# Kernel tuning notes

Measured on AMD Instinct MI355X. Metric: run time of the kernel, lower is better.

Reference implementation:

```python
import jax, jax.numpy as jnp
import numpy as np

K_NEIGS = 3
M_PROB = 1.0
EPS = 1e-12


def _gen_G_single(ft):
    """Build normalized hypergraph Laplacian G [N,N] from node coords ft [N,3].

    Mirrors construct_H_with_KNN (is_probH=True, m_prob=1) + generate_G_from_H
    from the HGNN reference code: per-center KNN hyperedges with probabilistic
    incidence exp(-d^2/(m_prob*avg_d)^2), then G = Dv^-1/2 H De^-1 H^T Dv^-1/2.
    """
    N = ft.shape[0]
    # squared pairwise Euclidean distances [N,N]
    sq_norm = jnp.sum(ft * ft, axis=1)
    sq = jnp.maximum(sq_norm[:, None] + sq_norm[None, :] - 2.0 * ft @ ft.T, 0.0)
    dist = jnp.sqrt(sq + EPS)
    avg_dis = jnp.mean(dist, axis=1)  # per-center mean distance [N]
    # K nearest neighbors per center (self is always included: sq[c,c]=0)
    neg_sq, idx = jax.lax.top_k(-sq, K_NEIGS)  # [N,K]
    # prob incidence: exp(-d^2 / (m_prob*avg)^2); neg_sq = -d^2
    vals = jnp.exp(neg_sq / (M_PROB * avg_dis[:, None]) ** 2)  # [N,K]
    # H[node, edge]: column c holds the K neighbors of center c
    H = jnp.zeros((N, N), ft.dtype).at[idx, jnp.arange(N)[:, None]].set(vals)
    de = jnp.sum(H, axis=0)              # edge degrees [N]
    dv = jnp.sum(H, axis=1)              # vertex degrees [N]
    inv_de = 1.0 / de
    dv2 = dv ** -0.5
    HW = H * inv_de[None, :]
    G = (dv2[:, None] * (HW @ H.T)) * dv2[None, :]
    return G


def reference(x, W1, b1, Wc, bc):
    # gen_G: per-batch hypergraph G [B,N,N]
    G = jax.vmap(_gen_G_single)(x)
    # HGNN_conv with both args = G: out = G @ (G @ W1 + b1)  -> [B,N,H1]
    f = jnp.matmul(G, jnp.matmul(G, W1) + b1)
    # max-pool over nodes, then classifier
    f = jnp.max(f, axis=1)               # [B,H1]
    return f @ Wc + bc                   # [B,class_num]


def setup_inputs() -> dict:
    key = jax.random.key(0)
    k1, k2, k3, k4, k5 = jax.random.split(key, 5)
    B, N, H1, C = 4, 2048, 128, 8
    x = jax.random.normal(k1, (B, N, 3), dtype=jnp.float32)
    W1 = jax.random.normal(k2, (N, H1), dtype=jnp.float32) / np.sqrt(N)
    b1 = jax.random.normal(k3, (H1,), dtype=jnp.float32) * 0.01
    Wc = jax.random.normal(k4, (H1, C), dtype=jnp.float32) / np.sqrt(H1)
    bc = jax.random.normal(k5, (C,), dtype=jnp.float32) * 0.01
    return {"x": x, "W1": W1, "b1": b1, "Wc": Wc, "bc": bc}
```

## Files before the change

kernel.cpp:

```cpp
#include <hip/hip_runtime.h>
#include <math.h>

#define NN 2048
#define BB 4
#define HD 128
#define CNUM 8
#define WPB 4
#define CAP 64
#define CAPG 128
#define NPB 4

typedef unsigned long long u64;

__device__ __forceinline__ u64 pack_key(float sq, int j) {
    return ((u64)__float_as_uint(sq) << 32) | (unsigned)j;
}
__device__ __forceinline__ void ins3(u64 k, u64& k0, u64& k1, u64& k2) {
    u64 a = k  < k2 ? k  : k2;
    u64 b = k0 > a  ? k0 : a;
    k0    = k0 < a  ? k0 : a;
    k2    = k1 > b  ? k1 : b;
    k1    = k1 < b  ? k1 : b;
}

__global__ void k_prep(const float* __restrict__ x, float4* __restrict__ pts) {
    const int t = blockIdx.x * 256 + threadIdx.x;
    const float a = x[3 * t], c = x[3 * t + 1], d = x[3 * t + 2];
    pts[t] = make_float4(a, c, d, a * a + c * c + d * d);
}

__global__ __launch_bounds__(256) void k_dist(
        const float4* __restrict__ pts,
        int* __restrict__ idx, float* __restrict__ vals,
        float* __restrict__ de, float* __restrict__ dv,
        int* __restrict__ cnt, int2* __restrict__ rev) {
    const int b = blockIdx.y;
    const float4* pb = pts + b * NN;
    const int wave = threadIdx.x >> 6;
    const int lane = threadIdx.x & 63;
    const int i = blockIdx.x * WPB + wave;
    const float4 ci = pb[i];
    u64 k0 = ~0ull, k1 = ~0ull, k2 = ~0ull;
    float dsA = 0.f, dsB = 0.f;
    for (int t = lane; t < NN; t += 256) {
        const float4 pa = pb[t];
        const float4 pv = pb[t + 64];
        const float4 pc = pb[t + 128];
        const float4 pd = pb[t + 192];
        const float qa = fmaxf(ci.w + pa.w - 2.0f * (ci.x * pa.x + ci.y * pa.y + ci.z * pa.z), 0.0f);
        const float qb = fmaxf(ci.w + pv.w - 2.0f * (ci.x * pv.x + ci.y * pv.y + ci.z * pv.z), 0.0f);
        const float qc = fmaxf(ci.w + pc.w - 2.0f * (ci.x * pc.x + ci.y * pc.y + ci.z * pc.z), 0.0f);
        const float qd = fmaxf(ci.w + pd.w - 2.0f * (ci.x * pd.x + ci.y * pd.y + ci.z * pd.z), 0.0f);
        dsA += __builtin_amdgcn_sqrtf(qa + 1e-12f) + __builtin_amdgcn_sqrtf(qc + 1e-12f);
        dsB += __builtin_amdgcn_sqrtf(qb + 1e-12f) + __builtin_amdgcn_sqrtf(qd + 1e-12f);
        ins3(pack_key(qa, t),       k0, k1, k2);
        ins3(pack_key(qb, t + 64),  k0, k1, k2);
        ins3(pack_key(qc, t + 128), k0, k1, k2);
        ins3(pack_key(qd, t + 192), k0, k1, k2);
    }
    float dsum = dsA + dsB;
    for (int off = 32; off > 0; off >>= 1) {
        const u64 o0 = __shfl_xor(k0, off);
        const u64 o1 = __shfl_xor(k1, off);
        const u64 o2 = __shfl_xor(k2, off);
        dsum += __shfl_xor(dsum, off);
        ins3(o0, k0, k1, k2);
        ins3(o1, k0, k1, k2);
        ins3(o2, k0, k1, k2);
    }
    if (lane == 0) {
        const float s0 = __uint_as_float((unsigned)(k0 >> 32));
        const float s1 = __uint_as_float((unsigned)(k1 >> 32));
        const float s2 = __uint_as_float((unsigned)(k2 >> 32));
        const int   i0 = (int)(k0 & 0xffffffffu);
        const int   i1 = (int)(k1 & 0xffffffffu);
        const int   i2 = (int)(k2 & 0xffffffffu);
        const float avg = dsum * (1.0f / NN);
        const float inva2 = 1.0f / (avg * avg);
        const float v0 = expf(-s0 * inva2);
        const float v1 = expf(-s1 * inva2);
        const float v2 = expf(-s2 * inva2);
        const int base = (b * NN + i) * 3;
        idx[base] = i0; idx[base + 1] = i1; idx[base + 2] = i2;
        vals[base] = v0; vals[base + 1] = v1; vals[base + 2] = v2;
        de[b * NN + i] = v0 + v1 + v2;
        atomicAdd(&dv[b * NN + i0], v0);
        atomicAdd(&dv[b * NN + i1], v1);
        atomicAdd(&dv[b * NN + i2], v2);
        const int p0 = atomicAdd(&cnt[b * NN + i0], 1);
        if (p0 < CAP) rev[((size_t)(b * NN + i0)) * CAP + p0] = make_int2(i, __float_as_int(v0));
        const int p1 = atomicAdd(&cnt[b * NN + i1], 1);
        if (p1 < CAP) rev[((size_t)(b * NN + i1)) * CAP + p1] = make_int2(i, __float_as_int(v1));
        const int p2 = atomicAdd(&cnt[b * NN + i2], 1);
        if (p2 < CAP) rev[((size_t)(b * NN + i2)) * CAP + p2] = make_int2(i, __float_as_int(v2));
    }
}

__global__ void k_gbuild(const int* __restrict__ idx, const float* __restrict__ vals,
                         const float* __restrict__ de, const float* __restrict__ dv,
                         const int* __restrict__ cnt, const int2* __restrict__ rev,
                         int2* __restrict__ glist, int* __restrict__ gn) {
    const int b = blockIdx.y;
    const int i = blockIdx.x * 256 + threadIdx.x;
    const int ni = b * NN + i;
    const int cn = min(cnt[ni], CAP);
    const float wi = rsqrtf(dv[ni]);
    int m = 0;
    for (int s = 0; s < cn; ++s) {
        const int2 r = rev[(size_t)ni * CAP + s];
        const int e = r.x;
        const float coef = wi * __int_as_float(r.y) / de[b * NN + e];
        const int eb = (b * NN + e) * 3;
        #pragma unroll
        for (int t = 0; t < 3; ++t) {
            const int j = idx[eb + t];
            const float gv = coef * vals[eb + t] * rsqrtf(dv[b * NN + j]);
            if (m < CAPG) glist[(size_t)ni * CAPG + m] = make_int2(j, __float_as_int(gv));
            ++m;
        }
    }
    gn[ni] = min(m, CAPG);
}

__global__ __launch_bounds__(256) void k_conv1(
        const float* __restrict__ W1, const float* __restrict__ b1,
        const int2* __restrict__ glist, const int* __restrict__ gn,
        float* __restrict__ f1) {
    const int b = blockIdx.y;
    const int i = blockIdx.x * 2 + (threadIdx.x >> 7);
    const int h = threadIdx.x & (HD - 1);
    const int ni = b * NN + i;
    const int n = gn[ni];
    const int2* gl = glist + (size_t)ni * CAPG;
    float acc = b1[h];
    int2 cur = gl[0];
    for (int s = 0; s < n; ++s) {
        const int2 nxt = gl[min(s + 1, n - 1)];
        acc += __int_as_float(cur.y) * W1[cur.x * HD + h];
        cur = nxt;
    }
    f1[(size_t)ni * HD + h] = acc;
}

__global__ __launch_bounds__(256) void k_conv2(
        const int2* __restrict__ glist, const int* __restrict__ gn,
        const float* __restrict__ f1, unsigned* __restrict__ pmaxK) {
    __shared__ float smx[2][HD];
    const int b = blockIdx.y;
    const int sub = threadIdx.x >> 7;
    const int h = threadIdx.x & (HD - 1);
    float mx = -INFINITY;
    for (int t = 0; t < NPB / 2; ++t) {
        const int i = blockIdx.x * NPB + t * 2 + sub;
        const int ni = b * NN + i;
        const int n = gn[ni];
        const int2* gl = glist + (size_t)ni * CAPG;
        float acc = 0.f;
        int2 cur = gl[0];
        for (int s = 0; s < n; ++s) {
            const int2 nxt = gl[min(s + 1, n - 1)];
            acc += __int_as_float(cur.y) * f1[((size_t)(b * NN + cur.x)) * HD + h];
            cur = nxt;
        }
        mx = fmaxf(mx, acc);
    }
    smx[sub][h] = mx;
    __syncthreads();
    if (sub == 0) {
        const float v = fmaxf(smx[0][h], smx[1][h]);
        unsigned u = __float_as_uint(v);
        u = (u & 0x80000000u) ? ~u : (u | 0x80000000u);
        atomicMax(&pmaxK[b * HD + h], u);
    }
}

__global__ void k_cls(const float* __restrict__ Wc, const float* __restrict__ bc,
                      const unsigned* __restrict__ pmaxK, float* __restrict__ out) {
    __shared__ float smax[HD];
    const int b = blockIdx.x, h = threadIdx.x;
    unsigned u = pmaxK[b * HD + h];
    u = (u & 0x80000000u) ? (u ^ 0x80000000u) : ~u;
    smax[h] = __uint_as_float(u);
    __syncthreads();
    if (h < CNUM) {
        float acc = bc[h];
        for (int q = 0; q < HD; ++q) acc += smax[q] * Wc[q * CNUM + h];
        out[b * CNUM + h] = acc;
    }
}

extern "C" void kernel_launch(void* const* d_in, const int* in_sizes, int n_in,
                              void* d_out, int out_size, void* d_ws, size_t ws_size,
                              hipStream_t stream) {
    const float* x  = (const float*)d_in[0];
    const float* W1 = (const float*)d_in[1];
    const float* b1 = (const float*)d_in[2];
    const float* Wc = (const float*)d_in[3];
    const float* bc = (const float*)d_in[4];
    float* out = (float*)d_out;

    float4*   pts   = (float4*)d_ws;
    float*    dv    = (float*)(pts + BB * NN);
    int*      cnt   = (int*)(dv + BB * NN);
    unsigned* pmaxK = (unsigned*)(cnt + BB * NN);
    float*    de    = (float*)(pmaxK + BB * HD);
    int*      idx   = (int*)(de + BB * NN);
    float*    vals  = (float*)(idx + BB * NN * 3);
    int*      gn    = (int*)(vals + BB * NN * 3);
    int2*     rev   = (int2*)(gn + BB * NN);
    int2*     glist = rev + (size_t)BB * NN * CAP;
    float*    f1    = (float*)(glist + (size_t)BB * NN * CAPG);

    hipMemsetAsync(dv, 0, (size_t)(2 * BB * NN + BB * HD) * sizeof(float), stream);

    k_prep  <<<BB * NN / 256, 256, 0, stream>>>(x, pts);
    k_dist  <<<dim3(NN / WPB, BB), 256, 0, stream>>>(pts, idx, vals, de, dv, cnt, rev);
    k_gbuild<<<dim3(NN / 256, BB), 256, 0, stream>>>(idx, vals, de, dv, cnt, rev, glist, gn);
    k_conv1 <<<dim3(NN / 2, BB), 256, 0, stream>>>(W1, b1, glist, gn, f1);
    k_conv2 <<<dim3(NN / NPB, BB), 256, 0, stream>>>(glist, gn, f1, pmaxK);
    k_cls   <<<BB, HD, 0, stream>>>(Wc, bc, pmaxK, out);
}
```

Before: 139.4 us.

## Factor G into H·De⁻¹·Hᵀ passes instead of building explicit G neighbor lists

```diff
diff --git a/kernel.cpp b/kernel.cpp
--- a/kernel.cpp
+++ b/kernel.cpp
@@ -7,7 +7,6 @@
 #define CNUM 8
 #define WPB 4
 #define CAP 64
-#define CAPG 128
 #define NPB 4
 
 typedef unsigned long long u64;
@@ -96,55 +95,67 @@
     }
 }
 
-__global__ void k_gbuild(const int* __restrict__ idx, const float* __restrict__ vals,
-                         const float* __restrict__ de, const float* __restrict__ dv,
-                         const int* __restrict__ cnt, const int2* __restrict__ rev,
-                         int2* __restrict__ glist, int* __restrict__ gn) {
-    const int b = blockIdx.y;
-    const int i = blockIdx.x * 256 + threadIdx.x;
-    const int ni = b * NN + i;
-    const int cn = min(cnt[ni], CAP);
-    const float wi = rsqrtf(dv[ni]);
-    int m = 0;
+__global__ __launch_bounds__(256) void k_edge1(
+        const float* __restrict__ W1, const int* __restrict__ idx,
+        const float* __restrict__ vals, const float* __restrict__ de,
+        const float* __restrict__ dv, float* __restrict__ P1) {
+    const int eg = blockIdx.x * 2 + (threadIdx.x >> 7);
+    const int h = threadIdx.x & (HD - 1);
+    const int b = eg >> 11;
+    const int base = eg * 3;
+    const int j0 = idx[base], j1 = idx[base + 1], j2 = idx[base + 2];
+    const float v0 = vals[base], v1 = vals[base + 1], v2 = vals[base + 2];
+    const float ide = 1.0f / de[eg];
+    const float g0 = v0 * rsqrtf(dv[b * NN + j0]);
+    const float g1 = v1 * rsqrtf(dv[b * NN + j1]);
+    const float g2 = v2 * rsqrtf(dv[b * NN + j2]);
+    P1[(size_t)eg * HD + h] =
+        ide * (g0 * W1[j0 * HD + h] + g1 * W1[j1 * HD + h] + g2 * W1[j2 * HD + h]);
+}
+
+__global__ __launch_bounds__(256) void k_node1(
+        const float* __restrict__ b1, const float* __restrict__ dv,
+        const int* __restrict__ cnt, const int2* __restrict__ rev,
+        const float* __restrict__ P1, float* __restrict__ f1) {
+    const int ig = blockIdx.x * 2 + (threadIdx.x >> 7);
+    const int h = threadIdx.x & (HD - 1);
+    const int b = ig >> 11;
+    const int cn = min(cnt[ig], CAP);
+    const int2* rl = rev + (size_t)ig * CAP;
+    float acc = 0.f;
+    int2 cur = rl[0];
     for (int s = 0; s < cn; ++s) {
-        const int2 r = rev[(size_t)ni * CAP + s];
-        const int e = r.x;
-        const float coef = wi * __int_as_float(r.y) / de[b * NN + e];
-        const int eb = (b * NN + e) * 3;
-        #pragma unroll
-        for (int t = 0; t < 3; ++t) {
-            const int j = idx[eb + t];
-            const float gv = coef * vals[eb + t] * rsqrtf(dv[b * NN + j]);
-            if (m < CAPG) glist[(size_t)ni * CAPG + m] = make_int2(j, __float_as_int(gv));
-            ++m;
-        }
-    }
-    gn[ni] = min(m, CAPG);
-}
-
-__global__ __launch_bounds__(256) void k_conv1(
-        const float* __restrict__ W1, const float* __restrict__ b1,
-        const int2* __restrict__ glist, const int* __restrict__ gn,
-        float* __restrict__ f1) {
-    const int b = blockIdx.y;
-    const int i = blockIdx.x * 2 + (threadIdx.x >> 7);
-    const int h = threadIdx.x & (HD - 1);
-    const int ni = b * NN + i;
-    const int n = gn[ni];
-    const int2* gl = glist + (size_t)ni * CAPG;
-    float acc = b1[h];
-    int2 cur = gl[0];
-    for (int s = 0; s < n; ++s) {
-        const int2 nxt = gl[min(s + 1, n - 1)];
-        acc += __int_as_float(cur.y) * W1[cur.x * HD + h];
+        const int2 nxt = rl[min(s + 1, cn - 1)];
+        acc += __int_as_float(cur.y) * P1[((size_t)(b * NN + cur.x)) * HD + h];
         cur = nxt;
     }
-    f1[(size_t)ni * HD + h] = acc;
-}
-
-__global__ __launch_bounds__(256) void k_conv2(
-        const int2* __restrict__ glist, const int* __restrict__ gn,
-        const float* __restrict__ f1, unsigned* __restrict__ pmaxK) {
+    f1[(size_t)ig * HD + h] = rsqrtf(dv[ig]) * acc + b1[h];
+}
+
+__global__ __launch_bounds__(256) void k_edge2(
+        const float* __restrict__ f1, const int* __restrict__ idx,
+        const float* __restrict__ vals, const float* __restrict__ de,
+        const float* __restrict__ dv, float* __restrict__ P2) {
+    const int eg = blockIdx.x * 2 + (threadIdx.x >> 7);
+    const int h = threadIdx.x & (HD - 1);
+    const int b = eg >> 11;
+    const int base = eg * 3;
+    const int j0 = idx[base], j1 = idx[base + 1], j2 = idx[base + 2];
+    const float v0 = vals[base], v1 = vals[base + 1], v2 = vals[base + 2];
+    const float ide = 1.0f / de[eg];
+    const float g0 = v0 * rsqrtf(dv[b * NN + j0]);
+    const float g1 = v1 * rsqrtf(dv[b * NN + j1]);
+    const float g2 = v2 * rsqrtf(dv[b * NN + j2]);
+    P2[(size_t)eg * HD + h] =
+        ide * (g0 * f1[((size_t)(b * NN + j0)) * HD + h]
+             + g1 * f1[((size_t)(b * NN + j1)) * HD + h]
+             + g2 * f1[((size_t)(b * NN + j2)) * HD + h]);
+}
+
+__global__ __launch_bounds__(256) void k_node2(
+        const float* __restrict__ dv, const int* __restrict__ cnt,
+        const int2* __restrict__ rev, const float* __restrict__ P2,
+        unsigned* __restrict__ pmaxK) {
     __shared__ float smx[2][HD];
     const int b = blockIdx.y;
     const int sub = threadIdx.x >> 7;
@@ -152,17 +163,17 @@
     float mx = -INFINITY;
     for (int t = 0; t < NPB / 2; ++t) {
         const int i = blockIdx.x * NPB + t * 2 + sub;
-        const int ni = b * NN + i;
-        const int n = gn[ni];
-        const int2* gl = glist + (size_t)ni * CAPG;
+        const int ig = b * NN + i;
+        const int cn = min(cnt[ig], CAP);
+        const int2* rl = rev + (size_t)ig * CAP;
         float acc = 0.f;
-        int2 cur = gl[0];
-        for (int s = 0; s < n; ++s) {
-            const int2 nxt = gl[min(s + 1, n - 1)];
-            acc += __int_as_float(cur.y) * f1[((size_t)(b * NN + cur.x)) * HD + h];
+        int2 cur = rl[0];
+        for (int s = 0; s < cn; ++s) {
+            const int2 nxt = rl[min(s + 1, cn - 1)];
+            acc += __int_as_float(cur.y) * P2[((size_t)(b * NN + cur.x)) * HD + h];
             cur = nxt;
         }
-        mx = fmaxf(mx, acc);
+        mx = fmaxf(mx, rsqrtf(dv[ig]) * acc);
     }
     smx[sub][h] = mx;
     __syncthreads();
@@ -206,17 +217,18 @@
     float*    de    = (float*)(pmaxK + BB * HD);
     int*      idx   = (int*)(de + BB * NN);
     float*    vals  = (float*)(idx + BB * NN * 3);
-    int*      gn    = (int*)(vals + BB * NN * 3);
-    int2*     rev   = (int2*)(gn + BB * NN);
-    int2*     glist = rev + (size_t)BB * NN * CAP;
-    float*    f1    = (float*)(glist + (size_t)BB * NN * CAPG);
+    int2*     rev   = (int2*)(vals + BB * NN * 3);
+    float*    P1    = (float*)(rev + (size_t)BB * NN * CAP);
+    float*    f1    = P1 + (size_t)BB * NN * HD;
+    float*    P2    = f1 + (size_t)BB * NN * HD;
 
     hipMemsetAsync(dv, 0, (size_t)(2 * BB * NN + BB * HD) * sizeof(float), stream);
 
-    k_prep  <<<BB * NN / 256, 256, 0, stream>>>(x, pts);
-    k_dist  <<<dim3(NN / WPB, BB), 256, 0, stream>>>(pts, idx, vals, de, dv, cnt, rev);
-    k_gbuild<<<dim3(NN / 256, BB), 256, 0, stream>>>(idx, vals, de, dv, cnt, rev, glist, gn);
-    k_conv1 <<<dim3(NN / 2, BB), 256, 0, stream>>>(W1, b1, glist, gn, f1);
-    k_conv2 <<<dim3(NN / NPB, BB), 256, 0, stream>>>(glist, gn, f1, pmaxK);
-    k_cls   <<<BB, HD, 0, stream>>>(Wc, bc, pmaxK, out);
-}
+    k_prep <<<BB * NN / 256, 256, 0, stream>>>(x, pts);
+    k_dist <<<dim3(NN / WPB, BB), 256, 0, stream>>>(pts, idx, vals, de, dv, cnt, rev);
+    k_edge1<<<BB * NN / 2, 256, 0, stream>>>(W1, idx, vals, de, dv, P1);
+    k_node1<<<BB * NN / 2, 256, 0, stream>>>(b1, dv, cnt, rev, P1, f1);
+    k_edge2<<<BB * NN / 2, 256, 0, stream>>>(f1, idx, vals, de, dv, P2);
+    k_node2<<<dim3(NN / NPB, BB), 256, 0, stream>>>(dv, cnt, rev, P2, pmaxK);
+    k_cls  <<<BB, HD, 0, stream>>>(Wc, bc, pmaxK, out);
+}
```

Result: faster. 128.6 us (-7.7%).
